# Kernel tuning notes

Measured on AMD Instinct MI355X. Metric: run time of the kernel, lower is better.

Reference implementation:

```python
import jax, jax.numpy as jnp
import numpy as np

N_EMBD = 1024
N_HEAD = 16
B, T = 2, 2048

def setup_inputs() -> dict:
    key = jax.random.key(0)
    ks = jax.random.split(key, 5)
    s = 1.0 / np.sqrt(N_EMBD)
    return {
        'x': jax.random.normal(ks[0], (B, T, N_EMBD), jnp.float32),
        'W_attn': jax.random.normal(ks[1], (N_EMBD, 3 * N_EMBD), jnp.float32) * s,
        'b_attn': jax.random.normal(ks[2], (3 * N_EMBD,), jnp.float32) * 0.02,
        'W_proj': jax.random.normal(ks[3], (N_EMBD, N_EMBD), jnp.float32) * s,
        'b_proj': jax.random.normal(ks[4], (N_EMBD,), jnp.float32) * 0.02,
    }

def reference(x, W_attn, b_attn, W_proj, b_proj):
    Bx, Tx, C = x.shape
    H = N_HEAD
    D = C // H  # head dim
    qkv = x @ W_attn + b_attn                      # [B,T,3C]
    q, k, v = jnp.split(qkv, 3, axis=-1)
    # [B,T,C] -> [B,H,T,D]
    q = q.reshape(Bx, Tx, H, D).transpose(0, 2, 1, 3)
    k = k.reshape(Bx, Tx, H, D).transpose(0, 2, 1, 3)
    v = v.reshape(Bx, Tx, H, D).transpose(0, 2, 1, 3)
    scale = 1.0 / jnp.sqrt(jnp.asarray(D, x.dtype))
    scores = jnp.einsum('bhqd,bhkd->bhqk', q, k) * scale   # [B,H,T,T]
    causal = jnp.tril(jnp.ones((Tx, Tx), bool))
    scores = jnp.where(causal, scores, jnp.asarray(-jnp.inf, scores.dtype))
    attn = jax.nn.softmax(scores, axis=-1)
    y = jnp.einsum('bhqk,bhkd->bhqd', attn, v)              # [B,H,T,D]
    y = y.transpose(0, 2, 1, 3).reshape(Bx, Tx, C)
    return y @ W_proj + b_proj
```

## Files before the change

kernel.cpp:

```cpp
#include <hip/hip_runtime.h>
#include <stdint.h>

typedef float f32x4 __attribute__((ext_vector_type(4)));
typedef float f32x16 __attribute__((ext_vector_type(16)));
typedef __bf16 bf16x8 __attribute__((ext_vector_type(8)));
typedef unsigned short ushort8 __attribute__((ext_vector_type(8)));
typedef unsigned int uint4v __attribute__((ext_vector_type(4)));
typedef unsigned short u16;

#define DEVINL static __device__ __forceinline__

#define EXP2(x) exp2f(x)

#define VMCNT(N)                                          \
  {                                                       \
    asm volatile("s_waitcnt vmcnt(" #N ")" ::: "memory"); \
    __builtin_amdgcn_sched_barrier(0);                    \
  }

DEVINL void barrier_raw() {
  __builtin_amdgcn_sched_barrier(0);
  __builtin_amdgcn_s_barrier();
  __builtin_amdgcn_sched_barrier(0);
}

DEVINL u16 f2bf(float f) {
  __bf16 h = (__bf16)f;
  return __builtin_bit_cast(u16, h);
}

DEVINL unsigned cvtpk(float lo, float hi) {
  unsigned r;
  asm("v_cvt_pk_bf16_f32 %0, %1, %2" : "=v"(r) : "v"(lo), "v"(hi));
  return r;
}

DEVINL void plswap(unsigned& a, unsigned& b) {
  asm("v_permlane32_swap_b32 %0, %1" : "+v"(a), "+v"(b));
}

DEVINL void gload16(const void* g, void* l) {
  __builtin_amdgcn_global_load_lds((__attribute__((address_space(1))) void*)g,
                                   (__attribute__((address_space(3))) void*)l, 16, 0, 0);
}

DEVINL f32x4 mfma16(bf16x8 a, bf16x8 b, f32x4 c) {
  return __builtin_amdgcn_mfma_f32_16x16x32_bf16(a, b, c, 0, 0, 0);
}
DEVINL f32x16 mfma32(bf16x8 a, bf16x8 b, f32x16 c) {
  return __builtin_amdgcn_mfma_f32_32x32x16_bf16(a, b, c, 0, 0, 0);
}

__global__ __launch_bounds__(256) void k_prep(const float* __restrict__ x,
                                              u16* __restrict__ xb,
                                              const float* __restrict__ Wa,
                                              u16* __restrict__ WaT,
                                              const float* __restrict__ Wp,
                                              u16* __restrict__ WpT) {
  __shared__ float tile[32][33];
  const int bid = blockIdx.x;
  if (bid < 2048) {
    const int i = bid * 256 + threadIdx.x;
    const float4* p = (const float4*)x + (size_t)i * 2;
    float4 a = p[0], b = p[1];
    ushort8 o;
    o[0] = f2bf(a.x); o[1] = f2bf(a.y); o[2] = f2bf(a.z); o[3] = f2bf(a.w);
    o[4] = f2bf(b.x); o[5] = f2bf(b.y); o[6] = f2bf(b.z); o[7] = f2bf(b.w);
    *((ushort8*)xb + i) = o;
    return;
  }
  const float* in;
  u16* out;
  int C, cx, ry;
  if (bid < 5120) {
    const int bx = bid - 2048;
    in = Wa; out = WaT; C = 3072; cx = bx % 96; ry = bx / 96;
  } else {
    const int bx = bid - 5120;
    in = Wp; out = WpT; C = 1024; cx = bx & 31; ry = bx >> 5;
  }
  const int tx = threadIdx.x & 31, ty = threadIdx.x >> 5;
  const int c0 = cx * 32, r0 = ry * 32;
#pragma unroll
  for (int k = 0; k < 4; ++k)
    tile[ty + k * 8][tx] = in[(size_t)(r0 + ty + k * 8) * C + (c0 + tx)];
  __syncthreads();
#pragma unroll
  for (int k = 0; k < 4; ++k)
    out[(size_t)(c0 + ty + k * 8) * 1024 + (r0 + tx)] = f2bf(tile[tx][ty + k * 8]);
}

template <int ROWS>
DEVINL void stageRx64(const u16* __restrict__ g, int ld, u16* lds, int t) {
#pragma unroll
  for (int i = 0; i < ROWS / 32; ++i) {
    int ci = i * 256 + t;
    int row = ci >> 3, gr = ci & 7;
    int gs = gr ^ (row & 7);
    gload16(g + (size_t)row * ld + gs * 8, lds + ci * 8);
  }
}

template <int ROWS>
DEVINL void stageRx32(const u16* __restrict__ g, int ld, u16* lds, int t) {
#pragma unroll
  for (int i = 0; i < ROWS / 64; ++i) {
    int ci = i * 256 + t;
    int row = ci >> 2, gr = ci & 3;
    int gs = gr ^ ((row >> 1) & 3);
    gload16(g + (size_t)row * ld + gs * 8, lds + ci * 8);
  }
}

DEVINL void gemm_core_128b32(const u16* __restrict__ A, const u16* __restrict__ B,
                             int Kdim, u16* As, u16* Bs, int t, f32x4 acc[4][4]) {
  const int l = t & 63, lr = l & 15, lg = l >> 4;
  const int wr = t >> 7, wc = (t >> 6) & 1;
  const int nk = Kdim >> 5;
  stageRx32<128>(A, Kdim, As, t);
  stageRx32<128>(B, Kdim, Bs, t);
  for (int kt = 0; kt < nk; ++kt) {
    if (kt + 1 < nk) {
      stageRx32<128>(A + (kt + 1) * 32, Kdim, As + ((kt + 1) & 1) * 4096, t);
      stageRx32<128>(B + (kt + 1) * 32, Kdim, Bs + ((kt + 1) & 1) * 4096, t);
      VMCNT(4);
    } else {
      VMCNT(0);
    }
    barrier_raw();
    const u16* Asc = As + (kt & 1) * 4096;
    const u16* Bsc = Bs + (kt & 1) * 4096;
    bf16x8 af[4], bf[4];
#pragma unroll
    for (int mi = 0; mi < 4; ++mi) {
      int r = wr * 64 + mi * 16 + lr;
      int g = lg ^ ((r >> 1) & 3);
      af[mi] = *(const bf16x8*)(Asc + r * 32 + g * 8);
    }
#pragma unroll
    for (int ni = 0; ni < 4; ++ni) {
      int r = wc * 64 + ni * 16 + lr;
      int g = lg ^ ((r >> 1) & 3);
      bf[ni] = *(const bf16x8*)(Bsc + r * 32 + g * 8);
    }
#pragma unroll
    for (int mi = 0; mi < 4; ++mi)
#pragma unroll
      for (int ni = 0; ni < 4; ++ni)
        acc[mi][ni] = mfma16(af[mi], bf[ni], acc[mi][ni]);
    barrier_raw();
  }
}

DEVINL void gemm_core_64(const u16* __restrict__ A, const u16* __restrict__ B,
                         int Kdim, u16* As, u16* Bs, int t, f32x4 acc[2][4]) {
  const int l = t & 63, lr = l & 15, lg = l >> 4;
  const int wr = t >> 7, wc = (t >> 6) & 1;
  const int nk = Kdim >> 6;
  stageRx64<64>(A, Kdim, As, t);
  stageRx64<128>(B, Kdim, Bs, t);
  for (int kt = 0; kt < nk; ++kt) {
    if (kt + 1 < nk) {
      stageRx64<64>(A + (kt + 1) * 64, Kdim, As + ((kt + 1) & 1) * 4096, t);
      stageRx64<128>(B + (kt + 1) * 64, Kdim, Bs + ((kt + 1) & 1) * 8192, t);
      VMCNT(6);
    } else {
      VMCNT(0);
    }
    barrier_raw();
    const u16* Asc = As + (kt & 1) * 4096;
    const u16* Bsc = Bs + (kt & 1) * 8192;
#pragma unroll
    for (int ks = 0; ks < 2; ++ks) {
      bf16x8 af[2], bf[4];
#pragma unroll
      for (int mi = 0; mi < 2; ++mi) {
        int r = wr * 32 + mi * 16 + lr;
        int g = (ks * 4 + lg) ^ (r & 7);
        af[mi] = *(const bf16x8*)(Asc + r * 64 + g * 8);
      }
#pragma unroll
      for (int ni = 0; ni < 4; ++ni) {
        int r = wc * 64 + ni * 16 + lr;
        int g = (ks * 4 + lg) ^ (r & 7);
        bf[ni] = *(const bf16x8*)(Bsc + r * 64 + g * 8);
      }
#pragma unroll
      for (int mi = 0; mi < 2; ++mi)
#pragma unroll
        for (int ni = 0; ni < 4; ++ni)
          acc[mi][ni] = mfma16(af[mi], bf[ni], acc[mi][ni]);
    }
    barrier_raw();
  }
}

__global__ __launch_bounds__(256) void k_gemm_qkv(const u16* __restrict__ xb,
                                                  const u16* __restrict__ WaT,
                                                  const float* __restrict__ b_attn,
                                                  u16* __restrict__ Qo,
                                                  u16* __restrict__ Ko,
                                                  u16* __restrict__ Vto) {
  __shared__ u16 As[2 * 128 * 32], Bs[2 * 128 * 32];
  const int t = threadIdx.x;
  const int bid = blockIdx.x;
  const int xcd = bid & 7;
  const int j = bid >> 3;
  const int by = ((xcd >> 1) << 3) + (j & 7);
  const int bx = (xcd & 1) * 12 + (j >> 3);
  const int m0 = by * 128, n0 = bx * 128;
  f32x4 acc[4][4] = {};
  gemm_core_128b32(xb + (size_t)m0 * 1024, WaT + (size_t)n0 * 1024, 1024, As, Bs, t,
                   acc);
  const int l = t & 63, lr = l & 15, lg = l >> 4;
  const int wr = t >> 7, wc = (t >> 6) & 1;
#pragma unroll
  for (int ni = 0; ni < 4; ++ni) {
    const int gcol = n0 + wc * 64 + ni * 16 + lr;
    const int part = gcol >> 10;
    const int h = (gcol & 1023) >> 6, d = gcol & 63;
    const float bias = b_attn[gcol];
    if (part == 2) {
#pragma unroll
      for (int mi = 0; mi < 4; ++mi) {
        const int tt0 = m0 + wr * 64 + mi * 16 + lg * 4;
        const int bb = tt0 >> 11, tt = tt0 & 2047;
        ushort4 pk;
        pk.x = f2bf(acc[mi][ni][0] + bias);
        pk.y = f2bf(acc[mi][ni][1] + bias);
        pk.z = f2bf(acc[mi][ni][2] + bias);
        pk.w = f2bf(acc[mi][ni][3] + bias);
        *(ushort4*)(Vto + (size_t)(bb * 16 + h) * 131072 + (size_t)d * 2048 + tt) = pk;
      }
    } else {
      const float osc = (part == 0) ? 0.18033688f : 1.0f;
      u16* dst = (part == 0) ? Qo : Ko;
#pragma unroll
      for (int mi = 0; mi < 4; ++mi)
#pragma unroll
        for (int r = 0; r < 4; ++r) {
          const int grow = m0 + wr * 64 + mi * 16 + lg * 4 + r;
          const int bb = grow >> 11, tt = grow & 2047;
          dst[(size_t)((bb * 16 + h) * 2048 + tt) * 64 + d] =
              f2bf((acc[mi][ni][r] + bias) * osc);
        }
    }
  }
}

__global__ __launch_bounds__(256) void k_gemm_proj(const u16* __restrict__ Yb,
                                                   const u16* __restrict__ WpT,
                                                   const float* __restrict__ b_proj,
                                                   float* __restrict__ out) {
  __shared__ u16 As[2 * 64 * 64], Bs[2 * 128 * 64];
  const int t = threadIdx.x;
  const int m0 = blockIdx.y * 64, n0 = blockIdx.x * 128;
  f32x4 acc[2][4] = {};
  gemm_core_64(Yb + (size_t)m0 * 1024, WpT + (size_t)n0 * 1024, 1024, As, Bs, t, acc);
  const int l = t & 63, lr = l & 15, lg = l >> 4;
  const int wr = t >> 7, wc = (t >> 6) & 1;
#pragma unroll
  for (int ni = 0; ni < 4; ++ni) {
    const int gcol = n0 + wc * 64 + ni * 16 + lr;
    const float bias = b_proj[gcol];
#pragma unroll
    for (int mi = 0; mi < 2; ++mi)
#pragma unroll
      for (int r = 0; r < 4; ++r) {
        const int grow = m0 + wr * 32 + mi * 16 + lg * 4 + r;
        out[(size_t)grow * 1024 + gcol] = acc[mi][ni][r] + bias;
      }
  }
}

__global__ __launch_bounds__(1024, 4) void k_flash(const u16* __restrict__ Q,
                                                   const u16* __restrict__ K,
                                                   const u16* __restrict__ Vt,
                                                   u16* __restrict__ Y) {
  __shared__ u16 SM[2 * 9216 + 2 * 8704];
  u16* KsB = SM;
  u16* VsB = SM + 2 * 9216;
  float* Ms = (float*)SM;

  const int t = threadIdx.x, l = t & 63, w = t >> 6;
  const int ql = l & 31, hi = l >> 5;
  const int wq = w & 3, wk = w >> 2;
  const int bid = blockIdx.x;
  const int bh = (bid & 7) + 8 * ((bid >> 3) & 3);
  const int p = bid >> 5;
  const size_t base = (size_t)bh * 131072;
  const int b = bh >> 4, hh = bh & 15;
  const int srow = t >> 3, scol = t & 7;
  const int sd = t >> 4, sck = t & 15;

  for (int half = 0; half < 2; ++half) {
    const int qt = half ? 15 - p : p;
    const int nsteps = qt + 1;
    const int qbase = qt * 128 + wq * 32;
    const int qrow = qbase + ql;

    __syncthreads();

    bf16x8 qb[4];
#pragma unroll
    for (int m = 0; m < 4; ++m)
      qb[m] = *(const bf16x8*)(Q + base + (size_t)qrow * 64 + hi * 8 + 16 * m);

    {
      ushort8 kv = *(const ushort8*)(K + base + (size_t)srow * 64 + scol * 8);
      ushort8 vv = *(const ushort8*)(Vt + base + (size_t)sd * 2048 + sck * 8);
      *(ushort8*)(KsB + srow * 72 + scol * 8) = kv;
      *(ushort8*)(VsB + sd * 136 + sck * 8) = vv;
    }
    __syncthreads();

    f32x16 accO0 = {}, accO1 = {};
    float rs_lane = 0.f;
    const int krow = wk * 32 + ql;

    for (int n = 0; n < nsteps; ++n) {
      const u16* Kc = KsB + (n & 1) * 9216;
      const u16* Vc = VsB + (n & 1) * 8704;
      const bool more = (n + 1 < nsteps);
      ushort8 kv, vv;
      if (more) {
        kv = *(const ushort8*)(K + base + (size_t)((n + 1) * 128 + srow) * 64 + scol * 8);
        vv = *(const ushort8*)(Vt + base + (size_t)sd * 2048 + (n + 1) * 128 + sck * 8);
      }
      const int kbase = n * 128 + wk * 32;
      if (kbase <= qbase + 31) {
        f32x16 st = {};
        __builtin_amdgcn_s_setprio(1);
#pragma unroll
        for (int m = 0; m < 4; ++m) {
          bf16x8 ka = *(const bf16x8*)(Kc + krow * 72 + (hi + 2 * m) * 8);
          st = mfma32(ka, qb[m], st);
        }
        __builtin_amdgcn_s_setprio(0);
        if (kbase + 31 > qbase) {
#pragma unroll
          for (int r = 0; r < 16; ++r) {
            const int keyl = (r & 3) + 8 * (r >> 2) + 4 * hi;
            if (kbase + keyl > qrow) st[r] = -1e30f;
          }
        }
        float pp[16];
#pragma unroll
        for (int r = 0; r < 16; ++r) {
          pp[r] = EXP2(st[r]);
          rs_lane += pp[r];
        }
        unsigned uu[8];
#pragma unroll
        for (int i = 0; i < 8; ++i) uu[i] = cvtpk(pp[2 * i], pp[2 * i + 1]);
        plswap(uu[0], uu[2]);
        plswap(uu[1], uu[3]);
        plswap(uu[4], uu[6]);
        plswap(uu[5], uu[7]);
        uint4v w0 = {uu[0], uu[1], uu[2], uu[3]};
        uint4v w1 = {uu[4], uu[5], uu[6], uu[7]};
        bf16x8 pf0 = __builtin_bit_cast(bf16x8, w0);
        bf16x8 pf1 = __builtin_bit_cast(bf16x8, w1);
        __builtin_amdgcn_s_setprio(1);
        {
          bf16x8 va0 = *(const bf16x8*)(Vc + ql * 136 + (4 * wk + hi) * 8);
          bf16x8 va1 = *(const bf16x8*)(Vc + ql * 136 + (4 * wk + 2 + hi) * 8);
          accO0 = mfma32(va0, pf0, accO0);
          accO0 = mfma32(va1, pf1, accO0);
          bf16x8 vb0 = *(const bf16x8*)(Vc + (32 + ql) * 136 + (4 * wk + hi) * 8);
          bf16x8 vb1 = *(const bf16x8*)(Vc + (32 + ql) * 136 + (4 * wk + 2 + hi) * 8);
          accO1 = mfma32(vb0, pf0, accO1);
          accO1 = mfma32(vb1, pf1, accO1);
        }
        __builtin_amdgcn_s_setprio(0);
      }
      if (more) {
        u16* Kn = KsB + ((n + 1) & 1) * 9216;
        u16* Vn = VsB + ((n + 1) & 1) * 8704;
        *(ushort8*)(Kn + srow * 72 + scol * 8) = kv;
        *(ushort8*)(Vn + sd * 136 + sck * 8) = vv;
      }
      __syncthreads();
    }

    rs_lane += __shfl_xor(rs_lane, 32);

    {
      float* Mp = Ms + (size_t)(((wq * 2 + (wk >> 1)) * 64 + l)) * 33;
      if (wk & 1) {
#pragma unroll
        for (int i = 0; i < 16; ++i) Mp[i] = accO0[i];
#pragma unroll
        for (int i = 0; i < 16; ++i) Mp[16 + i] = accO1[i];
        Mp[32] = rs_lane;
      }
      __syncthreads();
      if (!(wk & 1)) {
#pragma unroll
        for (int i = 0; i < 16; ++i) accO0[i] += Mp[i];
#pragma unroll
        for (int i = 0; i < 16; ++i) accO1[i] += Mp[16 + i];
        rs_lane += Mp[32];
      }
      __syncthreads();
    }
    {
      float* Mp = Ms + (size_t)((wq * 64 + l)) * 33;
      if (wk == 2) {
#pragma unroll
        for (int i = 0; i < 16; ++i) Mp[i] = accO0[i];
#pragma unroll
        for (int i = 0; i < 16; ++i) Mp[16 + i] = accO1[i];
        Mp[32] = rs_lane;
      }
      __syncthreads();
      if (wk == 0) {
        const float inv = 1.0f / (rs_lane + Mp[32]);
        u16* yb = Y + ((size_t)(b * 2048 + qrow)) * 1024 + hh * 64;
#pragma unroll
        for (int rq = 0; rq < 4; ++rq) {
          const int d0 = 8 * rq + 4 * hi;
          ushort4 o4;
          o4.x = f2bf((accO0[rq * 4 + 0] + Mp[rq * 4 + 0]) * inv);
          o4.y = f2bf((accO0[rq * 4 + 1] + Mp[rq * 4 + 1]) * inv);
          o4.z = f2bf((accO0[rq * 4 + 2] + Mp[rq * 4 + 2]) * inv);
          o4.w = f2bf((accO0[rq * 4 + 3] + Mp[rq * 4 + 3]) * inv);
          *(ushort4*)(yb + d0) = o4;
        }
#pragma unroll
        for (int rq = 0; rq < 4; ++rq) {
          const int d0 = 32 + 8 * rq + 4 * hi;
          ushort4 o4;
          o4.x = f2bf((accO1[rq * 4 + 0] + Mp[16 + rq * 4 + 0]) * inv);
          o4.y = f2bf((accO1[rq * 4 + 1] + Mp[16 + rq * 4 + 1]) * inv);
          o4.z = f2bf((accO1[rq * 4 + 2] + Mp[16 + rq * 4 + 2]) * inv);
          o4.w = f2bf((accO1[rq * 4 + 3] + Mp[16 + rq * 4 + 3]) * inv);
          *(ushort4*)(yb + d0) = o4;
        }
      }
    }
  }
}

extern "C" void kernel_launch(void* const* d_in, const int* in_sizes, int n_in,
                              void* d_out, int out_size, void* d_ws, size_t ws_size,
                              hipStream_t stream) {
  const float* x      = (const float*)d_in[0];
  const float* W_attn = (const float*)d_in[1];
  const float* b_attn = (const float*)d_in[2];
  const float* W_proj = (const float*)d_in[3];
  const float* b_proj = (const float*)d_in[4];
  float* out = (float*)d_out;

  char* ws = (char*)d_ws;
  u16* xb  = (u16*)(ws);
  u16* WaT = (u16*)(ws + (8u  << 20));
  u16* WpT = (u16*)(ws + (14u << 20));
  u16* Qb  = (u16*)(ws + (16u << 20));
  u16* Kb  = (u16*)(ws + (24u << 20));
  u16* Vtb = (u16*)(ws + (32u << 20));
  u16* Yb  = (u16*)(ws + (40u << 20));

  k_prep<<<dim3(6144), dim3(256), 0, stream>>>(x, xb, W_attn, WaT, W_proj, WpT);
  k_gemm_qkv<<<dim3(768), dim3(256), 0, stream>>>(xb, WaT, b_attn, Qb, Kb, Vtb);
  k_flash<<<dim3(256), dim3(1024), 0, stream>>>(Qb, Kb, Vtb, Yb);
  k_gemm_proj<<<dim3(8, 64), dim3(256), 0, stream>>>(Yb, WpT, b_proj, out);
}
```

Before: 99.94 us.

## Fuse x fp32-to-bf16 conversion into QKV GEMM A-tile staging

Removes the separate x-to-bf16 conversion pass from the prep kernel. The QKV GEMM now loads fp32 x directly into registers, converts it to bf16 and writes the swizzled LDS tile, with register prefetch two k-steps ahead. B tiles still go through direct global-to-LDS loads, and the vmcnt waits are retuned for the mixed loads. This saves a full write and reread of the bf16 x buffer. In exchange, each GEMM block now reads fp32 x, twice the bytes, and does the conversion redundantly across the 24 column blocks.

```diff
diff --git a/kernel.cpp b/kernel.cpp
--- a/kernel.cpp
+++ b/kernel.cpp
@@ -18,6 +18,12 @@
     __builtin_amdgcn_sched_barrier(0);                    \
   }
 
+#define LGKM0()                                        \
+  {                                                    \
+    asm volatile("s_waitcnt lgkmcnt(0)" ::: "memory"); \
+    __builtin_amdgcn_sched_barrier(0);                 \
+  }
+
 DEVINL void barrier_raw() {
   __builtin_amdgcn_sched_barrier(0);
   __builtin_amdgcn_s_barrier();
@@ -51,32 +57,26 @@
   return __builtin_amdgcn_mfma_f32_32x32x16_bf16(a, b, c, 0, 0, 0);
 }
 
-__global__ __launch_bounds__(256) void k_prep(const float* __restrict__ x,
-                                              u16* __restrict__ xb,
-                                              const float* __restrict__ Wa,
+DEVINL ushort8 pk8(float4 v0, float4 v1) {
+  ushort8 o;
+  o[0] = f2bf(v0.x); o[1] = f2bf(v0.y); o[2] = f2bf(v0.z); o[3] = f2bf(v0.w);
+  o[4] = f2bf(v1.x); o[5] = f2bf(v1.y); o[6] = f2bf(v1.z); o[7] = f2bf(v1.w);
+  return o;
+}
+
+__global__ __launch_bounds__(256) void k_prep(const float* __restrict__ Wa,
                                               u16* __restrict__ WaT,
                                               const float* __restrict__ Wp,
                                               u16* __restrict__ WpT) {
   __shared__ float tile[32][33];
   const int bid = blockIdx.x;
-  if (bid < 2048) {
-    const int i = bid * 256 + threadIdx.x;
-    const float4* p = (const float4*)x + (size_t)i * 2;
-    float4 a = p[0], b = p[1];
-    ushort8 o;
-    o[0] = f2bf(a.x); o[1] = f2bf(a.y); o[2] = f2bf(a.z); o[3] = f2bf(a.w);
-    o[4] = f2bf(b.x); o[5] = f2bf(b.y); o[6] = f2bf(b.z); o[7] = f2bf(b.w);
-    *((ushort8*)xb + i) = o;
-    return;
-  }
   const float* in;
   u16* out;
   int C, cx, ry;
-  if (bid < 5120) {
-    const int bx = bid - 2048;
-    in = Wa; out = WaT; C = 3072; cx = bx % 96; ry = bx / 96;
+  if (bid < 3072) {
+    in = Wa; out = WaT; C = 3072; cx = bid % 96; ry = bid / 96;
   } else {
-    const int bx = bid - 5120;
+    const int bx = bid - 3072;
     in = Wp; out = WpT; C = 1024; cx = bx & 31; ry = bx >> 5;
   }
   const int tx = threadIdx.x & 31, ty = threadIdx.x >> 5;
@@ -112,18 +112,52 @@
   }
 }
 
-DEVINL void gemm_core_128b32(const u16* __restrict__ A, const u16* __restrict__ B,
-                             int Kdim, u16* As, u16* Bs, int t, f32x4 acc[4][4]) {
+DEVINL void gemm_core_qkv(const float* __restrict__ A, const u16* __restrict__ B,
+                          u16* As, u16* Bs, int t, f32x4 acc[4][4]) {
   const int l = t & 63, lr = l & 15, lg = l >> 4;
   const int wr = t >> 7, wc = (t >> 6) & 1;
-  const int nk = Kdim >> 5;
-  stageRx32<128>(A, Kdim, As, t);
-  stageRx32<128>(B, Kdim, Bs, t);
+  const int nk = 32;
+  const int r0_ = t >> 2, g0_ = t & 3;
+  const int r1_ = (t + 256) >> 2;
+  const int d0_ = r0_ * 32 + ((g0_ ^ ((r0_ >> 1) & 3)) * 8);
+  const int d1_ = r1_ * 32 + ((g0_ ^ ((r1_ >> 1) & 3)) * 8);
+  const float* Ap0 = A + (size_t)r0_ * 1024 + g0_ * 8;
+  const float* Ap1 = A + (size_t)r1_ * 1024 + g0_ * 8;
+
+  float4 a00, a01, a10, a11;
+  a00 = *(const float4*)(Ap0);
+  a01 = *(const float4*)(Ap0 + 4);
+  a10 = *(const float4*)(Ap1);
+  a11 = *(const float4*)(Ap1 + 4);
+  stageRx32<128>(B, 1024, Bs, t);
+  *(ushort8*)(As + d0_) = pk8(a00, a01);
+  *(ushort8*)(As + d1_) = pk8(a10, a11);
+  a00 = *(const float4*)(Ap0 + 32);
+  a01 = *(const float4*)(Ap0 + 36);
+  a10 = *(const float4*)(Ap1 + 32);
+  a11 = *(const float4*)(Ap1 + 36);
+  LGKM0();
+  VMCNT(4);
+  barrier_raw();
+
   for (int kt = 0; kt < nk; ++kt) {
     if (kt + 1 < nk) {
-      stageRx32<128>(A + (kt + 1) * 32, Kdim, As + ((kt + 1) & 1) * 4096, t);
-      stageRx32<128>(B + (kt + 1) * 32, Kdim, Bs + ((kt + 1) & 1) * 4096, t);
-      VMCNT(4);
+      const int nx = ((kt + 1) & 1) * 4096;
+      stageRx32<128>(B + (kt + 1) * 32, 1024, Bs + nx, t);
+      *(ushort8*)(As + nx + d0_) = pk8(a00, a01);
+      *(ushort8*)(As + nx + d1_) = pk8(a10, a11);
+    }
+    if (kt + 2 < nk) {
+      a00 = *(const float4*)(Ap0 + (kt + 2) * 32);
+      a01 = *(const float4*)(Ap0 + (kt + 2) * 32 + 4);
+      a10 = *(const float4*)(Ap1 + (kt + 2) * 32);
+      a11 = *(const float4*)(Ap1 + (kt + 2) * 32 + 4);
+    }
+    LGKM0();
+    if (kt + 2 < nk) {
+      VMCNT(6);
+    } else if (kt + 1 < nk) {
+      VMCNT(2);
     } else {
       VMCNT(0);
     }
@@ -195,7 +229,7 @@
   }
 }
 
-__global__ __launch_bounds__(256) void k_gemm_qkv(const u16* __restrict__ xb,
+__global__ __launch_bounds__(256) void k_gemm_qkv(const float* __restrict__ x,
                                                   const u16* __restrict__ WaT,
                                                   const float* __restrict__ b_attn,
                                                   u16* __restrict__ Qo,
@@ -210,8 +244,7 @@
   const int bx = (xcd & 1) * 12 + (j >> 3);
   const int m0 = by * 128, n0 = bx * 128;
   f32x4 acc[4][4] = {};
-  gemm_core_128b32(xb + (size_t)m0 * 1024, WaT + (size_t)n0 * 1024, 1024, As, Bs, t,
-                   acc);
+  gemm_core_qkv(x + (size_t)m0 * 1024, WaT + (size_t)n0 * 1024, As, Bs, t, acc);
   const int l = t & 63, lr = l & 15, lg = l >> 4;
   const int wr = t >> 7, wc = (t >> 6) & 1;
 #pragma unroll
@@ -453,7 +486,6 @@
   float* out = (float*)d_out;
 
   char* ws = (char*)d_ws;
-  u16* xb  = (u16*)(ws);
   u16* WaT = (u16*)(ws + (8u  << 20));
   u16* WpT = (u16*)(ws + (14u << 20));
   u16* Qb  = (u16*)(ws + (16u << 20));
@@ -461,8 +493,8 @@
   u16* Vtb = (u16*)(ws + (32u << 20));
   u16* Yb  = (u16*)(ws + (40u << 20));
 
-  k_prep<<<dim3(6144), dim3(256), 0, stream>>>(x, xb, W_attn, WaT, W_proj, WpT);
-  k_gemm_qkv<<<dim3(768), dim3(256), 0, stream>>>(xb, WaT, b_attn, Qb, Kb, Vtb);
+  k_prep<<<dim3(4096), dim3(256), 0, stream>>>(W_attn, WaT, W_proj, WpT);
+  k_gemm_qkv<<<dim3(768), dim3(256), 0, stream>>>(x, WaT, b_attn, Qb, Kb, Vtb);
   k_flash<<<dim3(256), dim3(1024), 0, stream>>>(Qb, Kb, Vtb, Yb);
   k_gemm_proj<<<dim3(8, 64), dim3(256), 0, stream>>>(Yb, WpT, b_proj, out);
 }
```

New measurement: 101.8 us. Within noise of the previous version (+1.9%).

## Split flash attention into one query tile per block with XOR-swizzled LDS

Applied to the files above, without the earlier changes.

The flash kernel previously had each block process two paired query tiles (p and 15-p) in sequence. Now it launches twice as many blocks, each handling a single query tile, which gives more parallelism and less per-block serial work. K/V shared-memory tiles drop their padding in favour of an XOR swizzle, shrinking LDS to 64KB. The cross-wave reduction is split into two 16-float halves so it fits in the smaller LDS, at the cost of extra barriers. Without the pairing, blocks have unequal amounts of work, so load balance now depends on how the scheduler distributes them.

```diff
diff --git a/kernel.cpp b/kernel.cpp
--- a/kernel.cpp
+++ b/kernel.cpp
@@ -277,9 +277,9 @@
                                                    const u16* __restrict__ K,
                                                    const u16* __restrict__ Vt,
                                                    u16* __restrict__ Y) {
-  __shared__ u16 SM[2 * 9216 + 2 * 8704];
+  __shared__ u16 SM[32768];
   u16* KsB = SM;
-  u16* VsB = SM + 2 * 9216;
+  u16* VsB = SM + 16384;
   float* Ms = (float*)SM;
 
   const int t = threadIdx.x, l = t & 63, w = t >> 6;
@@ -287,156 +287,177 @@
   const int wq = w & 3, wk = w >> 2;
   const int bid = blockIdx.x;
   const int bh = (bid & 7) + 8 * ((bid >> 3) & 3);
-  const int p = bid >> 5;
+  const int jj = (bid >> 5) & 7;
+  const int qt = (bid >> 8) ? (15 - jj) : jj;
   const size_t base = (size_t)bh * 131072;
   const int b = bh >> 4, hh = bh & 15;
   const int srow = t >> 3, scol = t & 7;
   const int sd = t >> 4, sck = t & 15;
-
-  for (int half = 0; half < 2; ++half) {
-    const int qt = half ? 15 - p : p;
-    const int nsteps = qt + 1;
-    const int qbase = qt * 128 + wq * 32;
-    const int qrow = qbase + ql;
-
-    __syncthreads();
-
-    bf16x8 qb[4];
-#pragma unroll
-    for (int m = 0; m < 4; ++m)
-      qb[m] = *(const bf16x8*)(Q + base + (size_t)qrow * 64 + hi * 8 + 16 * m);
-
-    {
-      ushort8 kv = *(const ushort8*)(K + base + (size_t)srow * 64 + scol * 8);
-      ushort8 vv = *(const ushort8*)(Vt + base + (size_t)sd * 2048 + sck * 8);
-      *(ushort8*)(KsB + srow * 72 + scol * 8) = kv;
-      *(ushort8*)(VsB + sd * 136 + sck * 8) = vv;
-    }
-    __syncthreads();
-
-    f32x16 accO0 = {}, accO1 = {};
-    float rs_lane = 0.f;
-    const int krow = wk * 32 + ql;
-
-    for (int n = 0; n < nsteps; ++n) {
-      const u16* Kc = KsB + (n & 1) * 9216;
-      const u16* Vc = VsB + (n & 1) * 8704;
-      const bool more = (n + 1 < nsteps);
-      ushort8 kv, vv;
-      if (more) {
-        kv = *(const ushort8*)(K + base + (size_t)((n + 1) * 128 + srow) * 64 + scol * 8);
-        vv = *(const ushort8*)(Vt + base + (size_t)sd * 2048 + (n + 1) * 128 + sck * 8);
-      }
-      const int kbase = n * 128 + wk * 32;
-      if (kbase <= qbase + 31) {
-        f32x16 st = {};
-        __builtin_amdgcn_s_setprio(1);
-#pragma unroll
-        for (int m = 0; m < 4; ++m) {
-          bf16x8 ka = *(const bf16x8*)(Kc + krow * 72 + (hi + 2 * m) * 8);
-          st = mfma32(ka, qb[m], st);
+  const int kdst = srow * 64 + ((scol ^ (srow & 7)) * 8);
+  const int vdst = sd * 128 + ((sck ^ (sd & 7)) * 8);
+
+  const int nsteps = qt + 1;
+  const int qbase = qt * 128 + wq * 32;
+  const int qrow = qbase + ql;
+
+  bf16x8 qb[4];
+#pragma unroll
+  for (int m = 0; m < 4; ++m)
+    qb[m] = *(const bf16x8*)(Q + base + (size_t)qrow * 64 + hi * 8 + 16 * m);
+
+  {
+    ushort8 kv = *(const ushort8*)(K + base + (size_t)srow * 64 + scol * 8);
+    ushort8 vv = *(const ushort8*)(Vt + base + (size_t)sd * 2048 + sck * 8);
+    *(ushort8*)(KsB + kdst) = kv;
+    *(ushort8*)(VsB + vdst) = vv;
+  }
+  __syncthreads();
+
+  f32x16 accO0 = {}, accO1 = {};
+  float rs_lane = 0.f;
+  const int krow = wk * 32 + ql;
+  const int kswz = krow & 7;
+  const int vswz0 = ql & 7;
+  const int vswz1 = (32 + ql) & 7;
+
+  for (int n = 0; n < nsteps; ++n) {
+    const u16* Kc = KsB + (n & 1) * 8192;
+    const u16* Vc = VsB + (n & 1) * 8192;
+    const bool more = (n + 1 < nsteps);
+    ushort8 kv, vv;
+    if (more) {
+      kv = *(const ushort8*)(K + base + (size_t)((n + 1) * 128 + srow) * 64 + scol * 8);
+      vv = *(const ushort8*)(Vt + base + (size_t)sd * 2048 + (n + 1) * 128 + sck * 8);
+    }
+    const int kbase = n * 128 + wk * 32;
+    if (kbase <= qbase + 31) {
+      f32x16 st = {};
+      __builtin_amdgcn_s_setprio(1);
+#pragma unroll
+      for (int m = 0; m < 4; ++m) {
+        bf16x8 ka = *(const bf16x8*)(Kc + krow * 64 + (((hi + 2 * m) ^ kswz) * 8));
+        st = mfma32(ka, qb[m], st);
+      }
+      __builtin_amdgcn_s_setprio(0);
+      if (kbase + 31 > qbase) {
+#pragma unroll
+        for (int r = 0; r < 16; ++r) {
+          const int keyl = (r & 3) + 8 * (r >> 2) + 4 * hi;
+          if (kbase + keyl > qrow) st[r] = -1e30f;
         }
-        __builtin_amdgcn_s_setprio(0);
-        if (kbase + 31 > qbase) {
-#pragma unroll
-          for (int r = 0; r < 16; ++r) {
-            const int keyl = (r & 3) + 8 * (r >> 2) + 4 * hi;
-            if (kbase + keyl > qrow) st[r] = -1e30f;
-          }
-        }
-        float pp[16];
-#pragma unroll
-        for (int r = 0; r < 16; ++r) {
-          pp[r] = EXP2(st[r]);
-          rs_lane += pp[r];
-        }
-        unsigned uu[8];
-#pragma unroll
-        for (int i = 0; i < 8; ++i) uu[i] = cvtpk(pp[2 * i], pp[2 * i + 1]);
-        plswap(uu[0], uu[2]);
-        plswap(uu[1], uu[3]);
-        plswap(uu[4], uu[6]);
-        plswap(uu[5], uu[7]);
-        uint4v w0 = {uu[0], uu[1], uu[2], uu[3]};
-        uint4v w1 = {uu[4], uu[5], uu[6], uu[7]};
-        bf16x8 pf0 = __builtin_bit_cast(bf16x8, w0);
-        bf16x8 pf1 = __builtin_bit_cast(bf16x8, w1);
-        __builtin_amdgcn_s_setprio(1);
-        {
-          bf16x8 va0 = *(const bf16x8*)(Vc + ql * 136 + (4 * wk + hi) * 8);
-          bf16x8 va1 = *(const bf16x8*)(Vc + ql * 136 + (4 * wk + 2 + hi) * 8);
-          accO0 = mfma32(va0, pf0, accO0);
-          accO0 = mfma32(va1, pf1, accO0);
-          bf16x8 vb0 = *(const bf16x8*)(Vc + (32 + ql) * 136 + (4 * wk + hi) * 8);
-          bf16x8 vb1 = *(const bf16x8*)(Vc + (32 + ql) * 136 + (4 * wk + 2 + hi) * 8);
-          accO1 = mfma32(vb0, pf0, accO1);
-          accO1 = mfma32(vb1, pf1, accO1);
-        }
-        __builtin_amdgcn_s_setprio(0);
-      }
-      if (more) {
-        u16* Kn = KsB + ((n + 1) & 1) * 9216;
-        u16* Vn = VsB + ((n + 1) & 1) * 8704;
-        *(ushort8*)(Kn + srow * 72 + scol * 8) = kv;
-        *(ushort8*)(Vn + sd * 136 + sck * 8) = vv;
-      }
-      __syncthreads();
-    }
-
-    rs_lane += __shfl_xor(rs_lane, 32);
-
-    {
-      float* Mp = Ms + (size_t)(((wq * 2 + (wk >> 1)) * 64 + l)) * 33;
-      if (wk & 1) {
-#pragma unroll
-        for (int i = 0; i < 16; ++i) Mp[i] = accO0[i];
-#pragma unroll
-        for (int i = 0; i < 16; ++i) Mp[16 + i] = accO1[i];
-        Mp[32] = rs_lane;
-      }
-      __syncthreads();
-      if (!(wk & 1)) {
-#pragma unroll
-        for (int i = 0; i < 16; ++i) accO0[i] += Mp[i];
-#pragma unroll
-        for (int i = 0; i < 16; ++i) accO1[i] += Mp[16 + i];
-        rs_lane += Mp[32];
-      }
-      __syncthreads();
-    }
-    {
-      float* Mp = Ms + (size_t)((wq * 64 + l)) * 33;
-      if (wk == 2) {
-#pragma unroll
-        for (int i = 0; i < 16; ++i) Mp[i] = accO0[i];
-#pragma unroll
-        for (int i = 0; i < 16; ++i) Mp[16 + i] = accO1[i];
-        Mp[32] = rs_lane;
-      }
-      __syncthreads();
-      if (wk == 0) {
-        const float inv = 1.0f / (rs_lane + Mp[32]);
-        u16* yb = Y + ((size_t)(b * 2048 + qrow)) * 1024 + hh * 64;
-#pragma unroll
-        for (int rq = 0; rq < 4; ++rq) {
-          const int d0 = 8 * rq + 4 * hi;
-          ushort4 o4;
-          o4.x = f2bf((accO0[rq * 4 + 0] + Mp[rq * 4 + 0]) * inv);
-          o4.y = f2bf((accO0[rq * 4 + 1] + Mp[rq * 4 + 1]) * inv);
-          o4.z = f2bf((accO0[rq * 4 + 2] + Mp[rq * 4 + 2]) * inv);
-          o4.w = f2bf((accO0[rq * 4 + 3] + Mp[rq * 4 + 3]) * inv);
-          *(ushort4*)(yb + d0) = o4;
-        }
-#pragma unroll
-        for (int rq = 0; rq < 4; ++rq) {
-          const int d0 = 32 + 8 * rq + 4 * hi;
-          ushort4 o4;
-          o4.x = f2bf((accO1[rq * 4 + 0] + Mp[16 + rq * 4 + 0]) * inv);
-          o4.y = f2bf((accO1[rq * 4 + 1] + Mp[16 + rq * 4 + 1]) * inv);
-          o4.z = f2bf((accO1[rq * 4 + 2] + Mp[16 + rq * 4 + 2]) * inv);
-          o4.w = f2bf((accO1[rq * 4 + 3] + Mp[16 + rq * 4 + 3]) * inv);
-          *(ushort4*)(yb + d0) = o4;
-        }
+      }
+      float pp[16];
+#pragma unroll
+      for (int r = 0; r < 16; ++r) {
+        pp[r] = EXP2(st[r]);
+        rs_lane += pp[r];
+      }
+      unsigned uu[8];
+#pragma unroll
+      for (int i = 0; i < 8; ++i) uu[i] = cvtpk(pp[2 * i], pp[2 * i + 1]);
+      plswap(uu[0], uu[2]);
+      plswap(uu[1], uu[3]);
+      plswap(uu[4], uu[6]);
+      plswap(uu[5], uu[7]);
+      uint4v w0 = {uu[0], uu[1], uu[2], uu[3]};
+      uint4v w1 = {uu[4], uu[5], uu[6], uu[7]};
+      bf16x8 pf0 = __builtin_bit_cast(bf16x8, w0);
+      bf16x8 pf1 = __builtin_bit_cast(bf16x8, w1);
+      __builtin_amdgcn_s_setprio(1);
+      {
+        bf16x8 va0 = *(const bf16x8*)(Vc + ql * 128 + (((4 * wk + hi) ^ vswz0) * 8));
+        bf16x8 va1 =
+            *(const bf16x8*)(Vc + ql * 128 + (((4 * wk + 2 + hi) ^ vswz0) * 8));
+        accO0 = mfma32(va0, pf0, accO0);
+        accO0 = mfma32(va1, pf1, accO0);
+        bf16x8 vb0 =
+            *(const bf16x8*)(Vc + (32 + ql) * 128 + (((4 * wk + hi) ^ vswz1) * 8));
+        bf16x8 vb1 =
+            *(const bf16x8*)(Vc + (32 + ql) * 128 + (((4 * wk + 2 + hi) ^ vswz1) * 8));
+        accO1 = mfma32(vb0, pf0, accO1);
+        accO1 = mfma32(vb1, pf1, accO1);
+      }
+      __builtin_amdgcn_s_setprio(0);
+    }
+    if (more) {
+      u16* Kn = KsB + ((n + 1) & 1) * 8192;
+      u16* Vn = VsB + ((n + 1) & 1) * 8192;
+      *(ushort8*)(Kn + kdst) = kv;
+      *(ushort8*)(Vn + vdst) = vv;
+    }
+    __syncthreads();
+  }
+
+  rs_lane += __shfl_xor(rs_lane, 32);
+
+  {
+    float* Mp = Ms + (size_t)(((wq * 2 + (wk >> 1)) * 64 + l)) * 17;
+    if (wk & 1) {
+#pragma unroll
+      for (int i = 0; i < 16; ++i) Mp[i] = accO0[i];
+      Mp[16] = rs_lane;
+    }
+    __syncthreads();
+    if (!(wk & 1)) {
+#pragma unroll
+      for (int i = 0; i < 16; ++i) accO0[i] += Mp[i];
+      rs_lane += Mp[16];
+    }
+    __syncthreads();
+    if (wk & 1) {
+#pragma unroll
+      for (int i = 0; i < 16; ++i) Mp[i] = accO1[i];
+    }
+    __syncthreads();
+    if (!(wk & 1)) {
+#pragma unroll
+      for (int i = 0; i < 16; ++i) accO1[i] += Mp[i];
+    }
+    __syncthreads();
+  }
+  {
+    float* Mp = Ms + (size_t)((wq * 64 + l)) * 17;
+    if (wk == 2) {
+#pragma unroll
+      for (int i = 0; i < 16; ++i) Mp[i] = accO0[i];
+      Mp[16] = rs_lane;
+    }
+    __syncthreads();
+    if (wk == 0) {
+#pragma unroll
+      for (int i = 0; i < 16; ++i) accO0[i] += Mp[i];
+      rs_lane += Mp[16];
+    }
+    __syncthreads();
+    if (wk == 2) {
+#pragma unroll
+      for (int i = 0; i < 16; ++i) Mp[i] = accO1[i];
+    }
+    __syncthreads();
+    if (wk == 0) {
+#pragma unroll
+      for (int i = 0; i < 16; ++i) accO1[i] += Mp[i];
+      const float inv = 1.0f / rs_lane;
+      u16* yb = Y + ((size_t)(b * 2048 + qrow)) * 1024 + hh * 64;
+#pragma unroll
+      for (int rq = 0; rq < 4; ++rq) {
+        const int d0 = 8 * rq + 4 * hi;
+        ushort4 o4;
+        o4.x = f2bf(accO0[rq * 4 + 0] * inv);
+        o4.y = f2bf(accO0[rq * 4 + 1] * inv);
+        o4.z = f2bf(accO0[rq * 4 + 2] * inv);
+        o4.w = f2bf(accO0[rq * 4 + 3] * inv);
+        *(ushort4*)(yb + d0) = o4;
+      }
+#pragma unroll
+      for (int rq = 0; rq < 4; ++rq) {
+        const int d0 = 32 + 8 * rq + 4 * hi;
+        ushort4 o4;
+        o4.x = f2bf(accO1[rq * 4 + 0] * inv);
+        o4.y = f2bf(accO1[rq * 4 + 1] * inv);
+        o4.z = f2bf(accO1[rq * 4 + 2] * inv);
+        o4.w = f2bf(accO1[rq * 4 + 3] * inv);
+        *(ushort4*)(yb + d0) = o4;
       }
     }
   }
@@ -463,6 +484,6 @@
 
   k_prep<<<dim3(6144), dim3(256), 0, stream>>>(x, xb, W_attn, WaT, W_proj, WpT);
   k_gemm_qkv<<<dim3(768), dim3(256), 0, stream>>>(xb, WaT, b_attn, Qb, Kb, Vtb);
-  k_flash<<<dim3(256), dim3(1024), 0, stream>>>(Qb, Kb, Vtb, Yb);
+  k_flash<<<dim3(512), dim3(1024), 0, stream>>>(Qb, Kb, Vtb, Yb);
   k_gemm_proj<<<dim3(8, 64), dim3(256), 0, stream>>>(Yb, WpT, b_proj, out);
 }
```

Result: no change. 101.6 us (+1.7%).
